# Kernel optimization log

Hardware: AMD Instinct MI355X
Metric: run time of the kernel (lower is better)

Reference implementation:

```python
import jax, jax.numpy as jnp
import numpy as np

B, DIM, H, W = 4, 512, 64, 64
HEADS = 8
MAX_FREQ = 10000.0


def _rope_cos_sin(h, w, head_dim, dtype):
    # 2D RoPE: first quarter of half_dim uses row position, second quarter uses col position
    half = head_dim // 2
    quarter = half // 2
    pos_h = jnp.arange(h, dtype=dtype)
    pos_w = jnp.arange(w, dtype=dtype)
    gh, gw = jnp.meshgrid(pos_h, pos_w, indexing='ij')
    pos = jnp.stack([gh.ravel(), gw.ravel()], axis=-1)  # [N, 2]
    freqs = 1.0 / (MAX_FREQ ** (jnp.arange(quarter, dtype=dtype) / quarter))  # [quarter]
    ang_x = pos[:, 0:1] * freqs  # [N, quarter]
    ang_y = pos[:, 1:2] * freqs  # [N, quarter]
    cos = jnp.concatenate([jnp.cos(ang_x), jnp.cos(ang_y)], axis=-1)  # [N, half]
    sin = jnp.concatenate([jnp.sin(ang_x), jnp.sin(ang_y)], axis=-1)  # [N, half]
    return cos, sin


def _apply_rope(x, cos, sin):
    # x: [B, heads, N, head_dim]; cos/sin: [N, head_dim//2]
    d = x.shape[-1] // 2
    x1, x2 = x[..., :d], x[..., d:]
    return jnp.concatenate([x1 * cos - x2 * sin, x1 * sin + x2 * cos], axis=-1)


def setup_inputs() -> dict:
    key = jax.random.key(0)
    kx, kq, kp = jax.random.split(key, 3)
    x = jax.random.normal(kx, (B, DIM, H, W), dtype=jnp.float32)
    w_qkv = jax.random.normal(kq, (3 * DIM, DIM), dtype=jnp.float32) * (DIM ** -0.5)
    w_proj = jax.random.normal(kp, (DIM, DIM), dtype=jnp.float32) * (DIM ** -0.5)
    return {"x": x, "w_qkv": w_qkv, "w_proj": w_proj}


def reference(x, w_qkv, w_proj):
    Bb, C, Hh, Ww = x.shape
    heads = HEADS
    hd = C // heads
    N = Hh * Ww
    # 1x1 conv (bias-free) == channel-wise linear
    qkv = jnp.einsum('bchw,oc->bohw', x, w_qkv)  # [B, 3C, H, W]
    qkv = qkv.reshape(Bb, 3, heads, hd, Hh, Ww).transpose(1, 0, 2, 4, 5, 3)  # [3, B, heads, H, W, hd]
    q = qkv[0].reshape(Bb, heads, N, hd)
    k = qkv[1].reshape(Bb, heads, N, hd)
    v = qkv[2].reshape(Bb, heads, N, hd)
    cos, sin = _rope_cos_sin(Hh, Ww, hd, x.dtype)
    q = _apply_rope(q, cos, sin)
    k = _apply_rope(k, cos, sin)
    scale = hd ** -0.5
    attn = jax.nn.softmax(jnp.einsum('bhnd,bhmd->bhnm', q, k) * scale, axis=-1)  # [B, heads, N, N]
    out = jnp.einsum('bhnm,bhmd->bhnd', attn, v)  # [B, heads, N, hd]
    out = out.reshape(Bb, heads, Hh, Ww, hd).transpose(0, 1, 4, 2, 3).reshape(Bb, C, Hh, Ww)
    return jnp.einsum('bchw,oc->bohw', out, w_proj)
```

## Files before the change

### kernel.cpp

```cpp
#include <hip/hip_runtime.h>
#include <math.h>

#define B_    4
#define CDIM  512
#define HEADS 8
#define HD    64
#define NN    4096
#define QSZ   ((size_t)B_*HEADS*NN*HD)
#define SCALE_Q 0.18033688011112042f

typedef __attribute__((ext_vector_type(8))) short short8;
typedef __attribute__((ext_vector_type(4))) float f32x4;
union U4S8 { uint4 u; short8 s; };

__device__ inline unsigned pk(float a, float b) {
    unsigned ua = __float_as_uint(a), ub = __float_as_uint(b);
    ua += 0x7FFFu + ((ua >> 16) & 1u);
    ub += 0x7FFFu + ((ub >> 16) & 1u);
    return (ua >> 16) | (ub & 0xFFFF0000u);
}
__device__ inline unsigned short bf16_1(float a) {
    unsigned ua = __float_as_uint(a);
    ua += 0x7FFFu + ((ua >> 16) & 1u);
    return (unsigned short)(ua >> 16);
}
__device__ inline unsigned cvtpk(float a, float b) {
    unsigned r;
    asm("v_cvt_pk_bf16_f32 %0, %1, %2" : "=v"(r) : "v"(a), "v"(b));
    return r;
}

__device__ inline void load_lds16(const unsigned short* g, unsigned short* l) {
    __builtin_amdgcn_global_load_lds(
        (const __attribute__((address_space(1))) unsigned int*)g,
        (__attribute__((address_space(3))) unsigned int*)l, 16, 0, 0);
}

__global__ void conv_w_kernel(const float* __restrict__ wq, const float* __restrict__ wp,
                              unsigned short* __restrict__ wqb, unsigned short* __restrict__ wpb) {
    int id = blockIdx.x * 256 + threadIdx.x;
    const float* src; unsigned short* dst; size_t off; float sc = 1.0f;
    if (id < 98304) { src = wq; dst = wqb; off = (size_t)id * 8; if (off < 262144) sc = SCALE_Q; }
    else            { src = wp; dst = wpb; off = (size_t)(id - 98304) * 8; }
    float4 a = *(const float4*)(src + off);
    float4 b = *(const float4*)(src + off + 4);
    uint4 u;
    u.x = pk(a.x * sc, a.y * sc); u.y = pk(a.z * sc, a.w * sc);
    u.z = pk(b.x * sc, b.y * sc); u.w = pk(b.z * sc, b.w * sc);
    *(uint4*)(dst + off) = u;
}

__global__ void rope_table_kernel(float* __restrict__ ct, float* __restrict__ st) {
    int id = blockIdx.x * 256 + threadIdx.x;
    int j = id >> 12, n = id & 4095;
    int i = j & 15;
    float pos = (j < 16) ? (float)(n >> 6) : (float)(n & 63);
    float freq = exp2f(-(float)i * 0.8304820237218406f);
    float ang = pos * freq;
    ct[id] = cosf(ang);
    st[id] = sinf(ang);
}

__global__ __launch_bounds__(256) void transpose_x_kernel(
        const float* __restrict__ x, unsigned short* __restrict__ xt) {
    __shared__ unsigned short T[64 * 72];
    int t = threadIdx.x;
    int b = blockIdx.z, c0 = blockIdx.y * 64, n0 = blockIdx.x * 64;
    const float* xb = x + ((size_t)b * CDIM + c0) * NN + n0;
    int crow = t >> 2, nseg = t & 3;
#pragma unroll
    for (int g = 0; g < 4; ++g) {
        float4 f = *(const float4*)(xb + (size_t)crow * NN + nseg * 16 + g * 4);
        int nb = nseg * 16 + g * 4;
        T[(nb + 0) * 72 + crow] = bf16_1(f.x);
        T[(nb + 1) * 72 + crow] = bf16_1(f.y);
        T[(nb + 2) * 72 + crow] = bf16_1(f.z);
        T[(nb + 3) * 72 + crow] = bf16_1(f.w);
    }
    __syncthreads();
    unsigned short* xo = xt + ((size_t)b * NN + n0) * CDIM + c0;
    int nrow = t >> 2, cseg = t & 3;
    uint4 u0 = *(uint4*)(T + nrow * 72 + cseg * 16);
    uint4 u1 = *(uint4*)(T + nrow * 72 + cseg * 16 + 8);
    *(uint4*)(xo + (size_t)nrow * CDIM + cseg * 16)     = u0;
    *(uint4*)(xo + (size_t)nrow * CDIM + cseg * 16 + 8) = u1;
}

__global__ __launch_bounds__(256, 2) void qkv_mfma_kernel(
        const unsigned short* __restrict__ xt, const unsigned short* __restrict__ wq,
        unsigned short* __restrict__ qbf, unsigned short* __restrict__ kbf,
        unsigned short* __restrict__ vt,
        const float* __restrict__ ct, const float* __restrict__ st) {
    __shared__ unsigned short smem[8192];
    int t = threadIdx.x;
    int lane = t & 63, w = t >> 6;
    int qlo = lane & 15, quad = lane >> 4;
    int b = blockIdx.z, o0 = blockIdx.y * 128, n0 = blockIdx.x * 128;
    const unsigned short* xb = xt + (size_t)b * NN * CDIM;
    int row = t >> 2, seg = t & 3;
    int wn = (w & 1) * 64, wo = (w >> 1) * 64;

    f32x4 acc[4][4];
#pragma unroll
    for (int i = 0; i < 4; ++i)
#pragma unroll
        for (int j = 0; j < 4; ++j) acc[i][j] = f32x4{0.f, 0.f, 0.f, 0.f};

    for (int k0 = 0; k0 < 512; k0 += 32) {
        __syncthreads();
        load_lds16(xb + (size_t)(n0 + row) * 512 + k0 + seg * 8,        smem + t * 8);
        load_lds16(xb + (size_t)(n0 + 64 + row) * 512 + k0 + seg * 8,   smem + 2048 + t * 8);
        load_lds16(wq + (size_t)(o0 + row) * 512 + k0 + seg * 8,        smem + 4096 + t * 8);
        load_lds16(wq + (size_t)(o0 + 64 + row) * 512 + k0 + seg * 8,   smem + 6144 + t * 8);
        __syncthreads();
        U4S8 af[4], bf[4];
#pragma unroll
        for (int mt = 0; mt < 4; ++mt)
            af[mt].u = *(const uint4*)(smem + (wn + 16 * mt + qlo) * 32 + quad * 8);
#pragma unroll
        for (int nt = 0; nt < 4; ++nt)
            bf[nt].u = *(const uint4*)(smem + 4096 + (wo + 16 * nt + qlo) * 32 + quad * 8);
#pragma unroll
        for (int mt = 0; mt < 4; ++mt)
#pragma unroll
            for (int nt = 0; nt < 4; ++nt)
                acc[mt][nt] = __builtin_amdgcn_mfma_f32_16x16x32_bf16(
                    af[mt].s, bf[nt].s, acc[mt][nt], 0, 0, 0);
    }

    int og = o0 + wo;
    int s = og >> 9;
    int h = (og & 511) >> 6;
    int bh = b * HEADS + h;
    if (s < 2) {
        unsigned short* dst = (s ? kbf : qbf) + (size_t)bh * NN * HD;
#pragma unroll
        for (int mt = 0; mt < 4; ++mt) {
            int nbase = n0 + wn + 16 * mt + 4 * quad;
#pragma unroll
            for (int ntp = 0; ntp < 2; ++ntp) {
                int j = 16 * ntp + qlo;
                float4 c4 = *(const float4*)(ct + (size_t)j * NN + nbase);
                float4 s4 = *(const float4*)(st + (size_t)j * NN + nbase);
                float cc[4] = {c4.x, c4.y, c4.z, c4.w};
                float ss[4] = {s4.x, s4.y, s4.z, s4.w};
#pragma unroll
                for (int r = 0; r < 4; ++r) {
                    float x1 = acc[mt][ntp][r], x2 = acc[mt][ntp + 2][r];
                    size_t base = (size_t)(nbase + r) * HD;
                    dst[base + j]      = bf16_1(x1 * cc[r] - x2 * ss[r]);
                    dst[base + j + 32] = bf16_1(x1 * ss[r] + x2 * cc[r]);
                }
            }
        }
    } else {
        unsigned short* dst = vt + (size_t)bh * HD * NN;
#pragma unroll
        for (int mt = 0; mt < 4; ++mt)
#pragma unroll
            for (int nt = 0; nt < 4; ++nt) {
                int d = 16 * nt + qlo;
                int n = n0 + wn + 16 * mt + 4 * quad;
                uint2 u;
                u.x = pk(acc[mt][nt][0], acc[mt][nt][1]);
                u.y = pk(acc[mt][nt][2], acc[mt][nt][3]);
                *(uint2*)(dst + (size_t)d * NN + n) = u;
            }
    }
}

__global__ __launch_bounds__(256, 2) void attn_kernel(
        const unsigned short* __restrict__ qbf, const unsigned short* __restrict__ kbf,
        const unsigned short* __restrict__ vt, unsigned short* __restrict__ aot) {
    __shared__ unsigned char smem[18432];
    int t = threadIdx.x;
    int lane = t & 63, w = t >> 6;
    int qlo = lane & 15, quad = lane >> 4;
    int bb = blockIdx.z, hh = blockIdx.y;
    int bh = bb * HEADS + hh;
    int n0w = blockIdx.x * 256 + w * 64;

    U4S8 qf[4][2];
    const unsigned short* qg = qbf + ((size_t)bh * NN + n0w) * HD;
#pragma unroll
    for (int nt = 0; nt < 4; ++nt)
#pragma unroll
        for (int kt = 0; kt < 2; ++kt)
            qf[nt][kt].u = *(const uint4*)(qg + (size_t)(16 * nt + qlo) * 64 + 32 * kt + 8 * quad);

    short8 vone;
#pragma unroll
    for (int i = 0; i < 8; ++i) vone[i] = (short)0x3F80;

    f32x4 O[4][4];
#pragma unroll
    for (int mt = 0; mt < 4; ++mt)
#pragma unroll
        for (int nt = 0; nt < 4; ++nt) O[mt][nt] = f32x4{0.f, 0.f, 0.f, 0.f};
    f32x4 Lacc[4];
#pragma unroll
    for (int mt = 0; mt < 4; ++mt) Lacc[mt] = f32x4{0.f, 0.f, 0.f, 0.f};

    const uint4* kg = (const uint4*)kbf + (size_t)bh * NN * 8;
    const uint4* vg = (const uint4*)vt  + (size_t)bh * 64 * 512;

    int rr0 = t >> 3, s8 = t & 7;
    int voff = (s8 >> 2) * 64 + (s8 & 1) * 32 + ((s8 >> 1) & 1) * 8;
    uint4 kr0, kr1, vr0, vr1;
    kr0 = kg[(size_t)rr0 * 8 + s8];
    kr1 = kg[(size_t)(32 + rr0) * 8 + s8];
    vr0 = vg[(size_t)rr0 * 512 + s8];
    vr1 = vg[(size_t)(32 + rr0) * 512 + s8];

    for (int c = 0; c < NN / 64; ++c) {
        __syncthreads();
        *(uint4*)(smem + rr0 * 144 + s8 * 16)        = kr0;
        *(uint4*)(smem + (32 + rr0) * 144 + s8 * 16) = kr1;
        *(uint2*)(smem + 9216 + rr0 * 144 + voff)            = make_uint2(vr0.x, vr0.y);
        *(uint2*)(smem + 9216 + rr0 * 144 + voff + 16)       = make_uint2(vr0.z, vr0.w);
        *(uint2*)(smem + 9216 + (32 + rr0) * 144 + voff)     = make_uint2(vr1.x, vr1.y);
        *(uint2*)(smem + 9216 + (32 + rr0) * 144 + voff + 16)= make_uint2(vr1.z, vr1.w);
        __syncthreads();
        if (c + 1 < NN / 64) {
            int m0 = (c + 1) * 64;
            kr0 = kg[(size_t)(m0 + rr0) * 8 + s8];
            kr1 = kg[(size_t)(m0 + 32 + rr0) * 8 + s8];
            vr0 = vg[(size_t)rr0 * 512 + (m0 >> 3) + s8];
            vr1 = vg[(size_t)(32 + rr0) * 512 + (m0 >> 3) + s8];
        }

        f32x4 S[4][4];
#pragma unroll
        for (int mt = 0; mt < 4; ++mt)
#pragma unroll
            for (int nt = 0; nt < 4; ++nt) S[mt][nt] = f32x4{0.f, 0.f, 0.f, 0.f};
#pragma unroll
        for (int kt = 0; kt < 2; ++kt) {
            U4S8 ka[4];
#pragma unroll
            for (int mt = 0; mt < 4; ++mt)
                ka[mt].u = *(const uint4*)(smem + (16 * mt + qlo) * 144 + kt * 64 + quad * 16);
            __builtin_amdgcn_s_setprio(1);
#pragma unroll
            for (int nt = 0; nt < 4; ++nt)
#pragma unroll
                for (int mt = 0; mt < 4; ++mt)
                    S[mt][nt] = __builtin_amdgcn_mfma_f32_16x16x32_bf16(
                        ka[mt].s, qf[nt][kt].s, S[mt][nt], 0, 0, 0);
            __builtin_amdgcn_s_setprio(0);
        }

        uint2 pd[4][4];
#pragma unroll
        for (int nt = 0; nt < 4; ++nt)
#pragma unroll
            for (int mt = 0; mt < 4; ++mt) {
                f32x4 s4 = S[mt][nt];
                float p0 = __builtin_amdgcn_exp2f(s4[0]);
                float p1 = __builtin_amdgcn_exp2f(s4[1]);
                float p2 = __builtin_amdgcn_exp2f(s4[2]);
                float p3 = __builtin_amdgcn_exp2f(s4[3]);
                pd[nt][mt] = make_uint2(cvtpk(p0, p1), cvtpk(p2, p3));
            }

#pragma unroll
        for (int kt = 0; kt < 2; ++kt) {
            U4S8 pa[4];
#pragma unroll
            for (int mtP = 0; mtP < 4; ++mtP)
                pa[mtP].u = make_uint4(pd[mtP][2 * kt].x, pd[mtP][2 * kt].y,
                                       pd[mtP][2 * kt + 1].x, pd[mtP][2 * kt + 1].y);
            __builtin_amdgcn_s_setprio(1);
#pragma unroll
            for (int mtP = 0; mtP < 4; ++mtP)
                Lacc[mtP] = __builtin_amdgcn_mfma_f32_16x16x32_bf16(
                    pa[mtP].s, vone, Lacc[mtP], 0, 0, 0);
#pragma unroll
            for (int nt = 0; nt < 4; ++nt) {
                U4S8 vb;
                vb.u = *(const uint4*)(smem + 9216 + (16 * nt + qlo) * 144 + kt * 64 + quad * 16);
#pragma unroll
                for (int mtP = 0; mtP < 4; ++mtP)
                    O[mtP][nt] = __builtin_amdgcn_mfma_f32_16x16x32_bf16(
                        pa[mtP].s, vb.s, O[mtP][nt], 0, 0, 0);
            }
            __builtin_amdgcn_s_setprio(0);
        }
    }

    __syncthreads();
    unsigned short* Tw = (unsigned short*)(smem + w * 4608);
    unsigned short* aob = aot + ((size_t)bb * NN) * CDIM + hh * 64;
#pragma unroll
    for (int mt = 0; mt < 4; ++mt) {
        float iv[4];
#pragma unroll
        for (int r = 0; r < 4; ++r) iv[r] = 1.0f / Lacc[mt][r];
#pragma unroll
        for (int nt = 0; nt < 4; ++nt)
#pragma unroll
            for (int r = 0; r < 4; ++r)
                Tw[(4 * quad + r) * 72 + 16 * nt + qlo] = bf16_1(O[mt][nt][r] * iv[r]);
        int row = lane >> 2, cseg = lane & 3;
        uint4 u0 = *(uint4*)(Tw + row * 72 + cseg * 16);
        uint4 u1 = *(uint4*)(Tw + row * 72 + cseg * 16 + 8);
        unsigned short* arow = aob + (size_t)(n0w + 16 * mt + row) * CDIM + cseg * 16;
        *(uint4*)(arow)     = u0;
        *(uint4*)(arow + 8) = u1;
    }
}

__global__ __launch_bounds__(256, 2) void proj_mfma_kernel(
        const unsigned short* __restrict__ aot, const unsigned short* __restrict__ wp,
        float* __restrict__ out) {
    __shared__ unsigned short smem[8192];
    int t = threadIdx.x;
    int lane = t & 63, w = t >> 6;
    int qlo = lane & 15, quad = lane >> 4;
    int b = blockIdx.z, o0 = blockIdx.y * 128, n0 = blockIdx.x * 128;
    const unsigned short* ab = aot + (size_t)b * NN * CDIM;
    int row = t >> 2, seg = t & 3;
    int wn = (w & 1) * 64, wo = (w >> 1) * 64;

    f32x4 acc[4][4];
#pragma unroll
    for (int i = 0; i < 4; ++i)
#pragma unroll
        for (int j = 0; j < 4; ++j) acc[i][j] = f32x4{0.f, 0.f, 0.f, 0.f};

    for (int k0 = 0; k0 < 512; k0 += 32) {
        __syncthreads();
        load_lds16(ab + (size_t)(n0 + row) * 512 + k0 + seg * 8,        smem + t * 8);
        load_lds16(ab + (size_t)(n0 + 64 + row) * 512 + k0 + seg * 8,   smem + 2048 + t * 8);
        load_lds16(wp + (size_t)(o0 + row) * 512 + k0 + seg * 8,        smem + 4096 + t * 8);
        load_lds16(wp + (size_t)(o0 + 64 + row) * 512 + k0 + seg * 8,   smem + 6144 + t * 8);
        __syncthreads();
        U4S8 af[4], bf[4];
#pragma unroll
        for (int mt = 0; mt < 4; ++mt)
            af[mt].u = *(const uint4*)(smem + (wn + 16 * mt + qlo) * 32 + quad * 8);
#pragma unroll
        for (int nt = 0; nt < 4; ++nt)
            bf[nt].u = *(const uint4*)(smem + 4096 + (wo + 16 * nt + qlo) * 32 + quad * 8);
#pragma unroll
        for (int mt = 0; mt < 4; ++mt)
#pragma unroll
            for (int nt = 0; nt < 4; ++nt)
                acc[mt][nt] = __builtin_amdgcn_mfma_f32_16x16x32_bf16(
                    af[mt].s, bf[nt].s, acc[mt][nt], 0, 0, 0);
    }

    float* ob = out + (size_t)b * CDIM * NN;
#pragma unroll
    for (int mt = 0; mt < 4; ++mt)
#pragma unroll
        for (int nt = 0; nt < 4; ++nt) {
            int o = o0 + wo + 16 * nt + qlo;
            int n = n0 + wn + 16 * mt + 4 * quad;
            *(float4*)(ob + (size_t)o * NN + n) = *(float4*)&acc[mt][nt];
        }
}

extern "C" void kernel_launch(void* const* d_in, const int* in_sizes, int n_in,
                              void* d_out, int out_size, void* d_ws, size_t ws_size,
                              hipStream_t stream) {
    const float* x      = (const float*)d_in[0];
    const float* w_qkv  = (const float*)d_in[1];
    const float* w_proj = (const float*)d_in[2];
    float* out = (float*)d_out;
    unsigned short* ws = (unsigned short*)d_ws;

    unsigned short* xt  = ws;
    unsigned short* qbf = xt  + QSZ;
    unsigned short* kbf = qbf + QSZ;
    unsigned short* vt  = kbf + QSZ;
    unsigned short* aot = vt  + QSZ;
    unsigned short* wqb = aot + QSZ;
    unsigned short* wpb = wqb + 786432;
    float* ct = (float*)(wpb + 262144);
    float* st = ct + 32 * 4096;

    conv_w_kernel<<<512, 256, 0, stream>>>(w_qkv, w_proj, wqb, wpb);
    rope_table_kernel<<<512, 256, 0, stream>>>(ct, st);
    transpose_x_kernel<<<dim3(64, 8, B_), 256, 0, stream>>>(x, xt);
    qkv_mfma_kernel<<<dim3(32, 12, B_), 256, 0, stream>>>(xt, wqb, qbf, kbf, vt, ct, st);
    attn_kernel<<<dim3(NN / 256, HEADS, B_), 256, 0, stream>>>(qbf, kbf, vt, aot);
    proj_mfma_kernel<<<dim3(32, 4, B_), 256, 0, stream>>>(aot, wpb, out);
}
```

Measured before the change: 270.6 us.

## Switch attention kernel to 32x32x16 bf16 MFMA tiles

Rewrites the attention inner loop to use 32x32x16 MFMA instructions instead of 16x16x32. The K and V shared-memory fragment layouts, the V staging offsets, the P packing and the output transpose all change to match. The goal is fewer MFMA issues and fewer LDS fragment loads per FLOP. In exchange, each accumulator is 16 floats wide, so register pressure changes, and the S tile is now processed in two halves per chunk.

```diff
diff --git a/kernel.cpp b/kernel.cpp
--- a/kernel.cpp
+++ b/kernel.cpp
@@ -11,6 +11,7 @@
 
 typedef __attribute__((ext_vector_type(8))) short short8;
 typedef __attribute__((ext_vector_type(4))) float f32x4;
+typedef __attribute__((ext_vector_type(16))) float f32x16;
 union U4S8 { uint4 u; short8 s; };
 
 __device__ inline unsigned pk(float a, float b) {
@@ -175,37 +176,40 @@
     __shared__ unsigned char smem[18432];
     int t = threadIdx.x;
     int lane = t & 63, w = t >> 6;
-    int qlo = lane & 15, quad = lane >> 4;
+    int l31 = lane & 31, h = lane >> 5;
     int bb = blockIdx.z, hh = blockIdx.y;
     int bh = bb * HEADS + hh;
     int n0w = blockIdx.x * 256 + w * 64;
 
-    U4S8 qf[4][2];
+    U4S8 qf[2][4];
     const unsigned short* qg = qbf + ((size_t)bh * NN + n0w) * HD;
 #pragma unroll
-    for (int nt = 0; nt < 4; ++nt)
-#pragma unroll
-        for (int kt = 0; kt < 2; ++kt)
-            qf[nt][kt].u = *(const uint4*)(qg + (size_t)(16 * nt + qlo) * 64 + 32 * kt + 8 * quad);
+    for (int mtq = 0; mtq < 2; ++mtq)
+#pragma unroll
+        for (int ks = 0; ks < 4; ++ks)
+            qf[mtq][ks].u = *(const uint4*)(qg + (size_t)(32 * mtq + l31) * 64 + 16 * ks + 8 * h);
 
     short8 vone;
 #pragma unroll
     for (int i = 0; i < 8; ++i) vone[i] = (short)0x3F80;
 
-    f32x4 O[4][4];
-#pragma unroll
-    for (int mt = 0; mt < 4; ++mt)
-#pragma unroll
-        for (int nt = 0; nt < 4; ++nt) O[mt][nt] = f32x4{0.f, 0.f, 0.f, 0.f};
-    f32x4 Lacc[4];
-#pragma unroll
-    for (int mt = 0; mt < 4; ++mt) Lacc[mt] = f32x4{0.f, 0.f, 0.f, 0.f};
+    f32x16 Zv;
+#pragma unroll
+    for (int i = 0; i < 16; ++i) Zv[i] = 0.f;
+
+    f32x16 O[2][2];
+#pragma unroll
+    for (int mtq = 0; mtq < 2; ++mtq)
+#pragma unroll
+        for (int ntd = 0; ntd < 2; ++ntd) O[mtq][ntd] = Zv;
+    f32x16 Lacc[2];
+    Lacc[0] = Zv; Lacc[1] = Zv;
 
     const uint4* kg = (const uint4*)kbf + (size_t)bh * NN * 8;
     const uint4* vg = (const uint4*)vt  + (size_t)bh * 64 * 512;
 
     int rr0 = t >> 3, s8 = t & 7;
-    int voff = (s8 >> 2) * 64 + (s8 & 1) * 32 + ((s8 >> 1) & 1) * 8;
+    int voff = 32 * (s8 >> 1) + 8 * (s8 & 1);
     uint4 kr0, kr1, vr0, vr1;
     kr0 = kg[(size_t)rr0 * 8 + s8];
     kr1 = kg[(size_t)(32 + rr0) * 8 + s8];
@@ -216,10 +220,10 @@
         __syncthreads();
         *(uint4*)(smem + rr0 * 144 + s8 * 16)        = kr0;
         *(uint4*)(smem + (32 + rr0) * 144 + s8 * 16) = kr1;
-        *(uint2*)(smem + 9216 + rr0 * 144 + voff)            = make_uint2(vr0.x, vr0.y);
-        *(uint2*)(smem + 9216 + rr0 * 144 + voff + 16)       = make_uint2(vr0.z, vr0.w);
-        *(uint2*)(smem + 9216 + (32 + rr0) * 144 + voff)     = make_uint2(vr1.x, vr1.y);
-        *(uint2*)(smem + 9216 + (32 + rr0) * 144 + voff + 16)= make_uint2(vr1.z, vr1.w);
+        *(uint2*)(smem + 9216 + rr0 * 144 + voff)             = make_uint2(vr0.x, vr0.y);
+        *(uint2*)(smem + 9216 + rr0 * 144 + voff + 16)        = make_uint2(vr0.z, vr0.w);
+        *(uint2*)(smem + 9216 + (32 + rr0) * 144 + voff)      = make_uint2(vr1.x, vr1.y);
+        *(uint2*)(smem + 9216 + (32 + rr0) * 144 + voff + 16) = make_uint2(vr1.z, vr1.w);
         __syncthreads();
         if (c + 1 < NN / 64) {
             int m0 = (c + 1) * 64;
@@ -229,60 +233,57 @@
             vr1 = vg[(size_t)(32 + rr0) * 512 + (m0 >> 3) + s8];
         }
 
-        f32x4 S[4][4];
-#pragma unroll
-        for (int mt = 0; mt < 4; ++mt)
-#pragma unroll
-            for (int nt = 0; nt < 4; ++nt) S[mt][nt] = f32x4{0.f, 0.f, 0.f, 0.f};
-#pragma unroll
-        for (int kt = 0; kt < 2; ++kt) {
+#pragma unroll
+        for (int mtk = 0; mtk < 2; ++mtk) {
             U4S8 ka[4];
 #pragma unroll
-            for (int mt = 0; mt < 4; ++mt)
-                ka[mt].u = *(const uint4*)(smem + (16 * mt + qlo) * 144 + kt * 64 + quad * 16);
+            for (int ks = 0; ks < 4; ++ks)
+                ka[ks].u = *(const uint4*)(smem + (32 * mtk + l31) * 144 + 32 * ks + 16 * h);
+            f32x16 S[2];
             __builtin_amdgcn_s_setprio(1);
 #pragma unroll
-            for (int nt = 0; nt < 4; ++nt)
-#pragma unroll
-                for (int mt = 0; mt < 4; ++mt)
-                    S[mt][nt] = __builtin_amdgcn_mfma_f32_16x16x32_bf16(
-                        ka[mt].s, qf[nt][kt].s, S[mt][nt], 0, 0, 0);
+            for (int mtq = 0; mtq < 2; ++mtq) {
+                S[mtq] = __builtin_amdgcn_mfma_f32_32x32x16_bf16(
+                    ka[0].s, qf[mtq][0].s, Zv, 0, 0, 0);
+#pragma unroll
+                for (int ks = 1; ks < 4; ++ks)
+                    S[mtq] = __builtin_amdgcn_mfma_f32_32x32x16_bf16(
+                        ka[ks].s, qf[mtq][ks].s, S[mtq], 0, 0, 0);
+            }
             __builtin_amdgcn_s_setprio(0);
-        }
-
-        uint2 pd[4][4];
-#pragma unroll
-        for (int nt = 0; nt < 4; ++nt)
-#pragma unroll
-            for (int mt = 0; mt < 4; ++mt) {
-                f32x4 s4 = S[mt][nt];
-                float p0 = __builtin_amdgcn_exp2f(s4[0]);
-                float p1 = __builtin_amdgcn_exp2f(s4[1]);
-                float p2 = __builtin_amdgcn_exp2f(s4[2]);
-                float p3 = __builtin_amdgcn_exp2f(s4[3]);
-                pd[nt][mt] = make_uint2(cvtpk(p0, p1), cvtpk(p2, p3));
-            }
-
-#pragma unroll
-        for (int kt = 0; kt < 2; ++kt) {
-            U4S8 pa[4];
-#pragma unroll
-            for (int mtP = 0; mtP < 4; ++mtP)
-                pa[mtP].u = make_uint4(pd[mtP][2 * kt].x, pd[mtP][2 * kt].y,
-                                       pd[mtP][2 * kt + 1].x, pd[mtP][2 * kt + 1].y);
+
+            U4S8 pa[2][2];
+#pragma unroll
+            for (int mtq = 0; mtq < 2; ++mtq) {
+                float p[16];
+#pragma unroll
+                for (int r = 0; r < 16; ++r) p[r] = __builtin_amdgcn_exp2f(S[mtq][r]);
+#pragma unroll
+                for (int ksl = 0; ksl < 2; ++ksl) {
+                    pa[ksl][mtq].u.x = cvtpk(p[8 * ksl + 0], p[8 * ksl + 1]);
+                    pa[ksl][mtq].u.y = cvtpk(p[8 * ksl + 2], p[8 * ksl + 3]);
+                    pa[ksl][mtq].u.z = cvtpk(p[8 * ksl + 4], p[8 * ksl + 5]);
+                    pa[ksl][mtq].u.w = cvtpk(p[8 * ksl + 6], p[8 * ksl + 7]);
+                }
+            }
+
             __builtin_amdgcn_s_setprio(1);
 #pragma unroll
-            for (int mtP = 0; mtP < 4; ++mtP)
-                Lacc[mtP] = __builtin_amdgcn_mfma_f32_16x16x32_bf16(
-                    pa[mtP].s, vone, Lacc[mtP], 0, 0, 0);
-#pragma unroll
-            for (int nt = 0; nt < 4; ++nt) {
-                U4S8 vb;
-                vb.u = *(const uint4*)(smem + 9216 + (16 * nt + qlo) * 144 + kt * 64 + quad * 16);
-#pragma unroll
-                for (int mtP = 0; mtP < 4; ++mtP)
-                    O[mtP][nt] = __builtin_amdgcn_mfma_f32_16x16x32_bf16(
-                        pa[mtP].s, vb.s, O[mtP][nt], 0, 0, 0);
+            for (int ksl = 0; ksl < 2; ++ksl) {
+#pragma unroll
+                for (int mtq = 0; mtq < 2; ++mtq)
+                    Lacc[mtq] = __builtin_amdgcn_mfma_f32_32x32x16_bf16(
+                        pa[ksl][mtq].s, vone, Lacc[mtq], 0, 0, 0);
+#pragma unroll
+                for (int ntd = 0; ntd < 2; ++ntd) {
+                    U4S8 vb;
+                    vb.u = *(const uint4*)(smem + 9216 + (32 * ntd + l31) * 144
+                                           + 64 * mtk + 32 * ksl + 16 * h);
+#pragma unroll
+                    for (int mtq = 0; mtq < 2; ++mtq)
+                        O[mtq][ntd] = __builtin_amdgcn_mfma_f32_32x32x16_bf16(
+                            pa[ksl][mtq].s, vb.s, O[mtq][ntd], 0, 0, 0);
+                }
             }
             __builtin_amdgcn_s_setprio(0);
         }
@@ -292,21 +293,28 @@
     unsigned short* Tw = (unsigned short*)(smem + w * 4608);
     unsigned short* aob = aot + ((size_t)bb * NN) * CDIM + hh * 64;
 #pragma unroll
-    for (int mt = 0; mt < 4; ++mt) {
-        float iv[4];
-#pragma unroll
-        for (int r = 0; r < 4; ++r) iv[r] = 1.0f / Lacc[mt][r];
-#pragma unroll
-        for (int nt = 0; nt < 4; ++nt)
-#pragma unroll
-            for (int r = 0; r < 4; ++r)
-                Tw[(4 * quad + r) * 72 + 16 * nt + qlo] = bf16_1(O[mt][nt][r] * iv[r]);
-        int row = lane >> 2, cseg = lane & 3;
-        uint4 u0 = *(uint4*)(Tw + row * 72 + cseg * 16);
-        uint4 u1 = *(uint4*)(Tw + row * 72 + cseg * 16 + 8);
-        unsigned short* arow = aob + (size_t)(n0w + 16 * mt + row) * CDIM + cseg * 16;
-        *(uint4*)(arow)     = u0;
-        *(uint4*)(arow + 8) = u1;
+    for (int mtq = 0; mtq < 2; ++mtq) {
+        float iv[16];
+#pragma unroll
+        for (int r = 0; r < 16; ++r) iv[r] = 1.0f / Lacc[mtq][r];
+#pragma unroll
+        for (int rg = 0; rg < 2; ++rg) {
+#pragma unroll
+            for (int ntd = 0; ntd < 2; ++ntd)
+#pragma unroll
+                for (int rr = 0; rr < 8; ++rr) {
+                    int r = 8 * rg + rr;
+                    int q16 = (rr & 3) + 8 * (rr >> 2) + 4 * h;
+                    Tw[q16 * 72 + 32 * ntd + l31] = bf16_1(O[mtq][ntd][r] * iv[r]);
+                }
+            int row = lane >> 2, cseg = lane & 3;
+            uint4 u0 = *(uint4*)(Tw + row * 72 + cseg * 16);
+            uint4 u1 = *(uint4*)(Tw + row * 72 + cseg * 16 + 8);
+            unsigned short* arow = aob
+                + (size_t)(n0w + 32 * mtq + 16 * rg + row) * CDIM + cseg * 16;
+            *(uint4*)(arow)     = u0;
+            *(uint4*)(arow + 8) = u1;
+        }
     }
 }
 
```

Result: slower. 293.7 us (+8.5%).
